# Kernel optimization log

Hardware: AMD Instinct MI355X
Metric: run time of the kernel (lower is better)

## Reference

```python
import jax, jax.numpy as jnp
import numpy as np
import math

B, C, IMG, K, N = 8, 3, 512, 4, 4

# ---- Simoncelli steerable-pyramid radial/angular filters (frequency domain) ----

def _L(r):
    # lowpass raised-cosine: 2 for r<=pi/4, 0 for r>=pi/2
    rc = np.clip(r, np.pi / 4, np.pi / 2)
    return 2.0 * np.cos(np.pi / 2 * np.log2(4.0 * rc / np.pi))

def _Hf(r):
    # highpass raised-cosine: 0 for r<=pi/4, 1 for r>=pi/2
    rc = np.clip(r, np.pi / 4, np.pi / 2)
    return np.cos(np.pi / 2 * np.log2(2.0 * rc / np.pi))

def _grid(H):
    # fftshifted rows (u in [-pi,pi)), rfft half-spectrum cols (v in [0,pi])
    u = (np.arange(H) - H // 2) * (2.0 * np.pi / H)
    v = np.arange(H // 2 + 1) * (2.0 * np.pi / H)
    U, V = np.meshgrid(u, v, indexing='ij')
    return np.sqrt(U * U + V * V), np.arctan2(U, V)

def _make_filters():
    H = IMG
    r, _ = _grid(H)
    # HL0_matrix: stack of H0=H(r/2) and L0=L(r/2)/2  -> [2, H, H//2+1]
    hl0 = np.stack([_Hf(r / 2.0), _L(r / 2.0) / 2.0]).astype(np.float32)
    aK = 2.0 ** (K - 1) * math.factorial(K - 1) / math.sqrt(K * math.factorial(2 * (K - 1)))
    bs, ls = [], []
    for n in range(N):
        r, t = _grid(H)
        hr = _Hf(r)
        # B_matrix: B_k = H(r) * aK * cos(theta - pi*k/K)^(K-1), angle wrapped mod pi into [-pi/2,pi/2)
        b = np.stack([hr * aK * np.cos(np.mod(t - np.pi * k / K + np.pi / 2, np.pi) - np.pi / 2) ** (K - 1)
                      for k in range(K)])
        bs.append(b.astype(np.float32))
        # L_matrix_cropped / 4: central crop of L(r) matching central_crop(lf)
        ls.append((_L(r)[H // 4:H // 4 + H // 2, :H // 4 + 1] / 4.0)[None].astype(np.float32))
        H //= 2
    return hl0, bs, ls

def setup_inputs() -> dict:
    key = jax.random.key(0)
    x = jax.random.normal(key, (B, C, IMG, IMG), dtype=jnp.float32)
    hl0, bs, ls = _make_filters()
    d = {"x": x, "hl0": jnp.asarray(hl0)}
    for n in range(N):
        d[f"b{n}"] = jnp.asarray(bs[n])
        d[f"l{n}"] = jnp.asarray(ls[n])
    return d

def _central_crop(z):
    H = z.shape[-2]
    return z[..., H // 4:H // 4 + H // 2, :H // 4 + 1]

def _forward(x, hl0, bs, ls):
    # complex half-spectrum replaces torch's (real, imag) channel pair; filters are real
    X = jnp.fft.fftshift(jnp.fft.rfft2(x), axes=-2)[..., None, :, :]  # [B,C,1,H,Wh] c64
    Y = hl0 * X                                                       # [B,C,2,H,Wh]
    h0f = Y[..., 0:1, :, :]
    lf = Y[..., 1:2, :, :]
    outs = []
    for n in range(N):
        bf = bs[n] * lf                     # [B,C,K,Hn,Whn]
        lf = ls[n] * _central_crop(lf)      # [B,C,1,Hn/2,Hn/4+1]
        if n == 0:
            bf = jnp.concatenate([h0f, bf], axis=-3)  # prepend highpass residual
        outs.append(bf)
    outs.append(lf)
    res = []
    for o in outs:
        o = jnp.fft.ifftshift(o, axes=-2)
        Hn = o.shape[-2]
        res.append(jnp.fft.irfft2(o, s=(Hn, Hn)))     # [B,C,feat,Hn,Hn]
    # includeHF: split highpass channel out of level-0 bands
    res = [res[0][..., 0:1, :, :], res[0][..., 1:, :, :]] + res[1:]
    return tuple(r[:, None] for r in res)             # each [B,1,C,feat,Hn,Hn]

def reference(x, hl0, b0, b1, b2, b3, l0, l1, l2, l3):
    return _forward(x, hl0, [b0, b1, b2, b3], [l0, l1, l2, l3])
```

## Files before the change

kernel.cpp:

```cpp
#include <hip/hip_runtime.h>
#include <hip/hip_bf16.h>


#define PI_F 3.14159265358979323846f

static __device__ inline float2 f2add(float2 a, float2 b){ return make_float2(a.x+b.x, a.y+b.y); }
static __device__ inline float2 f2sub(float2 a, float2 b){ return make_float2(a.x-b.x, a.y-b.y); }
static __device__ inline float2 cmul(float2 a, float2 b){ return make_float2(a.x*b.x - a.y*b.y, a.x*b.y + a.y*b.x); }

template<int N, bool INV>
static __device__ inline void fill_tw(float2* tw, int tid) {
    for (int m = tid; m < N; m += 256) {
        float ang = (INV ? 2.0f * PI_F : -2.0f * PI_F) * (float)m / (float)N;
        float s, c; __sincosf(ang, &s, &c);
        tw[m] = make_float2(c, s);
    }
}

template<int N, int F, bool INV>
static __device__ float2* fft_lds(float2* bufa, float2* bufb, const float2* tw, int tid) {
    constexpr int L = (N==512)?9:(N==256)?8:(N==128)?7:(N==64)?6:5;
    float2* src = bufa;
    float2* dst = bufb;
    if constexpr (L & 1) {
        __syncthreads();
        constexpr int NB = F * (N/2);
#pragma unroll
        for (int qq = 0; qq < NB; qq += 256) {
            int q = qq + tid;
            int f = q / (N/2), j = q % (N/2);
            float2 u = src[f*N + j];
            float2 v = src[f*N + j + N/2];
            dst[f*N + 2*j]     = f2add(u, v);
            dst[f*N + 2*j + 1] = f2sub(u, v);
        }
        float2* t = src; src = dst; dst = t;
    }
    constexpr int S4 = L / 2;
    constexpr int NB4 = F * (N/4);
#pragma unroll
    for (int s = 0; s < S4; ++s) {
        const int Ns = ((L & 1) ? 2 : 1) << (2*s);
        __syncthreads();
#pragma unroll
        for (int qq = 0; qq < NB4; qq += 256) {
            int q = qq + tid;
            int f = q / (N/4), j = q % (N/4);
            int r = j & (Ns - 1);
            int m = r * (N / (4*Ns));
            float2 w1 = tw[m];
            float2 w2 = tw[(2*m) & (N-1)];
            float2 w3 = tw[(3*m) & (N-1)];
            const float2* sp = src + f*N + j;
            float2 c0 = sp[0];
            float2 c1 = cmul(w1, sp[N/4]);
            float2 c2 = cmul(w2, sp[2*(N/4)]);
            float2 c3 = cmul(w3, sp[3*(N/4)]);
            float2 t0 = f2add(c0, c2), t1 = f2sub(c0, c2);
            float2 t2 = f2add(c1, c3), d  = f2sub(c1, c3);
            float2 t3 = INV ? make_float2(-d.y, d.x) : make_float2(d.y, -d.x);
            float2* dp = dst + f*N + (((j - r) << 2) | r);
            dp[0]      = f2add(t0, t2);
            dp[Ns]     = f2add(t1, t3);
            dp[2*Ns]   = f2sub(t0, t2);
            dp[3*Ns]   = f2sub(t1, t3);
        }
        float2* t = src; src = dst; dst = t;
    }
    __syncthreads();
    return src;
}

__global__ __launch_bounds__(256) void k_fwd_rows(const float* __restrict__ x,
                                                  float2* __restrict__ S) {
    __shared__ float2 lds[2][2*512];
    __shared__ float2 tw[512];
    int bid = blockIdx.x;
    int i = bid / 128, p = bid % 128;
    int y0 = 4 * p;
    const float* rbase = x + ((size_t)(i*512 + y0)) * 512;
    int tid = threadIdx.x;
    fill_tw<512,false>(tw, tid);
    for (int t = tid; t < 1024; t += 256) {
        int f = t / 512, idx = t % 512;
        lds[0][f*512 + idx] = make_float2(rbase[(size_t)(2*f)*512 + idx],
                                          rbase[(size_t)(2*f+1)*512 + idx]);
    }
    float2* res = fft_lds<512,2,false>(&lds[0][0], &lds[1][0], tw, tid);
    for (int t = tid; t < 2*257; t += 256) {
        int f = t / 257, v = t % 257;
        float2 Zv = res[f*512 + v];
        float2 Zc = res[f*512 + ((512 - v) & 511)];
        float2* SA = S + ((size_t)(i*512 + y0 + 2*f)) * 257;
        SA[v]       = make_float2(0.5f*(Zv.x + Zc.x), 0.5f*(Zv.y - Zc.y));
        SA[257 + v] = make_float2(0.5f*(Zv.y + Zc.y), 0.5f*(Zc.x - Zv.x));
    }
}

template<int N, int CB>
__global__ __launch_bounds__(256) void k_fwd_cols(float2* __restrict__ S, int nTiles) {
    constexpr int W = N/2 + 1;
    __shared__ float2 lds[2][CB*N];
    __shared__ float2 tw[N];
    int tid = threadIdx.x, bid = blockIdx.x;
    int i = bid / nTiles, v0 = (bid % nTiles) * CB;
    fill_tw<N,false>(tw, tid);
    float2* base = S + (size_t)i * N * W;
    for (int q = tid; q < CB*N; q += 256) {
        int c = q % CB, r = q / CB, v = v0 + c;
        lds[0][c*N + r] = (v < W) ? base[(size_t)r*W + v] : make_float2(0.f, 0.f);
    }
    float2* res = fft_lds<N, CB, false>(&lds[0][0], &lds[1][0], tw, tid);
    for (int q = tid; q < CB*N; q += 256) {
        int c = q % CB, r = q / CB, v = v0 + c;
        if (v < W) base[(size_t)r*W + v] = res[c*N + r];
    }
}

__global__ void k_lfall(const float2* __restrict__ S, const float* __restrict__ hl0,
                        const float* __restrict__ l0, const float* __restrict__ l1,
                        const float* __restrict__ l2, const float* __restrict__ l3,
                        float2* __restrict__ LF1, float2* __restrict__ LF2,
                        float2* __restrict__ LF3, float2* __restrict__ LF4) {
    const int P1 = 256*129, P2 = 128*65, P3 = 64*33, P4 = 32*17;
    const int T1 = 24*P1, T2 = 24*P2, T3 = 24*P3, T4 = 24*P4;
    int idx = blockIdx.x * 256 + threadIdx.x;
    int lev, rem, perim; float2* dst;
    if (idx < T1)                { lev = 1; rem = idx;              perim = P1; dst = LF1; }
    else if (idx < T1+T2)        { lev = 2; rem = idx - T1;        perim = P2; dst = LF2; }
    else if (idx < T1+T2+T3)     { lev = 3; rem = idx - T1 - T2;   perim = P3; dst = LF3; }
    else if (idx < T1+T2+T3+T4)  { lev = 4; rem = idx - T1-T2-T3;  perim = P4; dst = LF4; }
    else return;
    int i = rem / perim;
    int off = rem % perim;
    int Hn = 512 >> lev, Wn = Hn/2 + 1;
    int u = off / Wn, v = off % Wn;
    float f = 1.0f;
    for (int m = lev - 1; m >= 0; --m) {
        int Hc = 512 >> (m + 1);
        int Wc = Hc/2 + 1;
        int s2 = (u + Hc/2) & (Hc - 1);
        const float* ls = (m==0) ? l0 : (m==1) ? l1 : (m==2) ? l2 : l3;
        f *= ls[s2 * Wc + v];
        int Hp = 512 >> m;
        u = (3*(Hp/4) + s2) & (Hp - 1);
    }
    f *= hl0[512*257 + (((u + 256) & 511) * 257 + v)];
    float2 sv = S[((size_t)i * 512 + u) * 257 + v];
    dst[(size_t)i * perim + off] = make_float2(sv.x * f, sv.y * f);
}

template<int N, int CB, int MODE>
__global__ __launch_bounds__(256) void k_inv_cols(
        const float2* __restrict__ specA, const float2* __restrict__ specB,
        const float* __restrict__ filtA, const float* __restrict__ filtB, int filtStride,
        const float* __restrict__ filtH,
        float2* __restrict__ Z, int chOff, int nTiles) {
    constexpr int W = N/2 + 1;
    __shared__ float2 lds[2][CB*N];
    __shared__ float2 tw[N];
    int tid = threadIdx.x, bid = blockIdx.x, y = blockIdx.y;
    int i = bid / nTiles, v0 = (bid % nTiles) * CB;
    fill_tw<N,true>(tw, tid);
    const float2* spec = (y == 0) ? specA : specB;
    const float* filt = nullptr;
    if (MODE >= 1) filt = (y == 0) ? filtA : filtB + (size_t)(y - chOff) * filtStride;
    const float2* base = spec + (size_t)i * N * W;
    float2* Zb = Z + ((size_t)y * 24 + i) * N * W;
    for (int q = tid; q < CB*N; q += 256) {
        int c = q % CB, r = q / CB, v = v0 + c;
        float2 val = make_float2(0.f, 0.f);
        if (v < W) {
            val = base[(size_t)r*W + v];
            if (MODE >= 1) {
                int fi = ((r + N/2) & (N-1)) * W + v;
                float f = filt[fi];
                if (MODE == 2 && y > 0) f *= filtH[fi];
                val.x *= f; val.y *= f;
            }
        }
        lds[0][c*N + r] = val;
    }
    float2* res = fft_lds<N, CB, true>(&lds[0][0], &lds[1][0], tw, tid);
    for (int q = tid; q < CB*N; q += 256) {
        int c = q % CB, r = q / CB, v = v0 + c;
        if (v < W) Zb[(size_t)r*W + v] = res[c*N + r];
    }
}

template<int N, int RB>
__global__ __launch_bounds__(256) void k_irfft_rows(
        const float2* __restrict__ Z,
        float* __restrict__ outA, int CHA,
        float* __restrict__ outB, int CHB, int chOff, int rowBlocks) {
    constexpr int W = N/2 + 1;
    __shared__ float2 lds[2][RB*N];
    __shared__ float2 tw[N];
    int tid = threadIdx.x, bid = blockIdx.x, y = blockIdx.y;
    int i = bid / rowBlocks, u0 = (bid % rowBlocks) * RB;
    fill_tw<N,true>(tw, tid);
    const float2* Zb = Z + ((size_t)y * 24 + i) * N * W;
    float* outb; int CH, ch;
    if (y == 0) { outb = outA; CH = CHA; ch = 0; }
    else        { outb = outB; CH = CHB; ch = y - chOff; }
    for (int q = tid; q < RB*N; q += 256) {
        int f = q / N, p = q % N;
        const float2* Zr = Zb + (size_t)(u0 + f) * W;
        float2 val;
        if (p == 0)          { float2 t = Zr[0];     val = make_float2(t.x, 0.f); }
        else if (p < N/2)    { val = Zr[p]; }
        else if (p == N/2)   { float2 t = Zr[N/2];   val = make_float2(t.x, 0.f); }
        else                 { float2 t = Zr[N - p]; val = make_float2(t.x, -t.y); }
        lds[0][f*N + p] = val;
    }
    float2* res = fft_lds<N, RB, true>(&lds[0][0], &lds[1][0], tw, tid);
    constexpr float sc = 1.0f / ((float)N * (float)N);
    for (int q = tid; q < RB*N; q += 256) {
        int f = q / N, p = q % N;
        int u = u0 + f;
        outb[(((size_t)i * CH + ch) * N + u) * N + p] = res[f*N + p].x * sc;
    }
}

extern "C" void kernel_launch(void* const* d_in, const int* in_sizes, int n_in,
                              void* d_out, int out_size, void* d_ws, size_t ws_size,
                              hipStream_t stream) {
    auto find = [&](int sz) -> const float* {
        for (int t = 0; t < n_in; ++t)
            if (in_sizes[t] == sz) return (const float*)d_in[t];
        return nullptr;
    };
    const float* x   = find(6291456);
    const float* hl0 = find(263168);
    const float* b0f = find(526336);
    const float* l0f = find(33024);
    const float* b1f = find(132096);
    const float* l1f = find(8320);
    const float* b2f = find(33280);
    const float* l2f = find(2112);
    const float* b3f = find(8448);
    const float* l3f = find(544);
    float* out = (float*)d_out;
    if (!x || !hl0 || !b0f || !l0f || !b1f || !l1f || !b2f || !l2f || !b3f || !l3f) return;

    const size_t P0 = (size_t)512*257, P1 = (size_t)256*129, P2 = (size_t)128*65,
                 P3 = (size_t)64*33,  P4 = (size_t)32*17;
    char* w = (char*)d_ws;
    float2* S   = (float2*)w; w += 24*P0*8;
    float2* LF1 = (float2*)w; w += 24*P1*8;
    float2* LF2 = (float2*)w; w += 24*P2*8;
    float2* LF3 = (float2*)w; w += 24*P3*8;
    float2* LF4 = (float2*)w; w += 24*P4*8;
    float2* Zar = (float2*)w; w += 5*24*P0*8;
    if ((size_t)(w - (char*)d_ws) > ws_size) return;

    const float* hl0_hi = hl0 + 512*257;

    k_fwd_rows<<<dim3(24*128), 256, 0, stream>>>(x, S);
    k_fwd_cols<512,4><<<dim3(24*65), 256, 0, stream>>>(S, 65);

    k_lfall<<<dim3(4125), 256, 0, stream>>>(S, hl0, l0f, l1f, l2f, l3f, LF1, LF2, LF3, LF4);

    k_inv_cols<512,4,2><<<dim3(24*65, 5), 256, 0, stream>>>(S, S, hl0, b0f, (int)P0, hl0_hi, Zar, 1, 65);
    k_irfft_rows<512,4><<<dim3(24*128, 5), 256, 0, stream>>>(Zar, out + 0, 1, out + 6291456, 4, 1, 128);

    k_inv_cols<256,8,1><<<dim3(24*17, 4), 256, 0, stream>>>(LF1, LF1, b1f, b1f, (int)P1, nullptr, Zar, 0, 17);
    k_irfft_rows<256,8><<<dim3(24*32, 4), 256, 0, stream>>>(Zar, out + 31457280, 4, out + 31457280, 4, 0, 32);

    k_inv_cols<128,16,1><<<dim3(24*5, 4), 256, 0, stream>>>(LF2, LF2, b2f, b2f, (int)P2, nullptr, Zar, 0, 5);
    k_irfft_rows<128,16><<<dim3(24*8, 4), 256, 0, stream>>>(Zar, out + 37748736, 4, out + 37748736, 4, 0, 8);

    k_inv_cols<64,32,1><<<dim3(24*2, 4), 256, 0, stream>>>(LF3, LF3, b3f, b3f, (int)P3, nullptr, Zar, 0, 2);
    k_irfft_rows<64,32><<<dim3(24*2, 4), 256, 0, stream>>>(Zar, out + 39321600, 4, out + 39321600, 4, 0, 2);

    k_inv_cols<32,64,0><<<dim3(24*1, 1), 256, 0, stream>>>(LF4, LF4, nullptr, nullptr, 0, nullptr, Zar, 0, 1);
    k_irfft_rows<32,32><<<dim3(24*1, 1), 256, 0, stream>>>(Zar, out + 39714816, 1, out + 39714816, 1, 0, 1);

    (void)out_size; (void)ws_size;
}
```

Before: 605.8 us.

## Use in-place padded LDS FFT, padded spectrum rows, and split level-0 inverse

Replaces the ping-pong LDS FFT with an in-place variant: each stage loads its operands into registers, synchronises, then writes back, using a padded LDS index (one extra slot every 16 elements) to reduce bank conflicts. Global spectrum rows are padded to 16-element-aligned widths (272, 144, ...) so column accesses line up better. Column FFT tiles are unified at 8 columns. The level-0 inverse is split into 3+2 channel launches so the Z scratch only needs 3 planes. The in-place FFT adds an extra barrier per stage and more registers, and the split adds launches.

```diff
diff --git a/kernel.cpp b/kernel.cpp
--- a/kernel.cpp
+++ b/kernel.cpp
@@ -7,6 +7,8 @@
 static __device__ inline float2 f2add(float2 a, float2 b){ return make_float2(a.x+b.x, a.y+b.y); }
 static __device__ inline float2 f2sub(float2 a, float2 b){ return make_float2(a.x-b.x, a.y-b.y); }
 static __device__ inline float2 cmul(float2 a, float2 b){ return make_float2(a.x*b.x - a.y*b.y, a.x*b.y + a.y*b.x); }
+
+#define PIDX(p) ((p) + ((p) >> 4))
 
 template<int N, bool INV>
 static __device__ inline void fill_tw(float2* tw, int tid) {
@@ -18,102 +20,131 @@
 }
 
 template<int N, int F, bool INV>
-static __device__ float2* fft_lds(float2* bufa, float2* bufb, const float2* tw, int tid) {
+static __device__ void fft_reg(float2* __restrict__ buf, const float2* __restrict__ tw, int tid) {
     constexpr int L = (N==512)?9:(N==256)?8:(N==128)?7:(N==64)?6:5;
-    float2* src = bufa;
-    float2* dst = bufb;
+    constexpr int STR = N + (N>>4) + 1;
     if constexpr (L & 1) {
+        constexpr int NB2 = F*(N/2);
+        constexpr int PT2 = (NB2 + 255)/256;
+        constexpr bool G2 = (NB2 % 256) != 0;
+        float2 ra[PT2], rb[PT2];
         __syncthreads();
-        constexpr int NB = F * (N/2);
-#pragma unroll
-        for (int qq = 0; qq < NB; qq += 256) {
-            int q = qq + tid;
-            int f = q / (N/2), j = q % (N/2);
-            float2 u = src[f*N + j];
-            float2 v = src[f*N + j + N/2];
-            dst[f*N + 2*j]     = f2add(u, v);
-            dst[f*N + 2*j + 1] = f2sub(u, v);
-        }
-        float2* t = src; src = dst; dst = t;
-    }
-    constexpr int S4 = L / 2;
-    constexpr int NB4 = F * (N/4);
+#pragma unroll
+        for (int t = 0; t < PT2; ++t) {
+            int q = t*256 + tid;
+            if (!G2 || q < NB2) {
+                int f = q / (N/2), j = q % (N/2);
+                ra[t] = buf[f*STR + PIDX(j)];
+                rb[t] = buf[f*STR + PIDX(j + N/2)];
+            }
+        }
+        __syncthreads();
+#pragma unroll
+        for (int t = 0; t < PT2; ++t) {
+            int q = t*256 + tid;
+            if (!G2 || q < NB2) {
+                int f = q / (N/2), j = q % (N/2);
+                buf[f*STR + PIDX(2*j)]   = f2add(ra[t], rb[t]);
+                buf[f*STR + PIDX(2*j+1)] = f2sub(ra[t], rb[t]);
+            }
+        }
+    }
+    constexpr int S4  = L/2;
+    constexpr int NB4 = F*(N/4);
+    constexpr int PT4 = (NB4 + 255)/256;
+    constexpr bool G4 = (NB4 % 256) != 0;
 #pragma unroll
     for (int s = 0; s < S4; ++s) {
         const int Ns = ((L & 1) ? 2 : 1) << (2*s);
+        float2 c0[PT4], c1[PT4], c2[PT4], c3[PT4];
         __syncthreads();
 #pragma unroll
-        for (int qq = 0; qq < NB4; qq += 256) {
-            int q = qq + tid;
-            int f = q / (N/4), j = q % (N/4);
-            int r = j & (Ns - 1);
-            int m = r * (N / (4*Ns));
-            float2 w1 = tw[m];
-            float2 w2 = tw[(2*m) & (N-1)];
-            float2 w3 = tw[(3*m) & (N-1)];
-            const float2* sp = src + f*N + j;
-            float2 c0 = sp[0];
-            float2 c1 = cmul(w1, sp[N/4]);
-            float2 c2 = cmul(w2, sp[2*(N/4)]);
-            float2 c3 = cmul(w3, sp[3*(N/4)]);
-            float2 t0 = f2add(c0, c2), t1 = f2sub(c0, c2);
-            float2 t2 = f2add(c1, c3), d  = f2sub(c1, c3);
-            float2 t3 = INV ? make_float2(-d.y, d.x) : make_float2(d.y, -d.x);
-            float2* dp = dst + f*N + (((j - r) << 2) | r);
-            dp[0]      = f2add(t0, t2);
-            dp[Ns]     = f2add(t1, t3);
-            dp[2*Ns]   = f2sub(t0, t2);
-            dp[3*Ns]   = f2sub(t1, t3);
-        }
-        float2* t = src; src = dst; dst = t;
+        for (int t = 0; t < PT4; ++t) {
+            int q = t*256 + tid;
+            if (!G4 || q < NB4) {
+                int f = q / (N/4), j = q % (N/4);
+                float2* b = buf + f*STR;
+                c0[t] = b[PIDX(j)];
+                c1[t] = b[PIDX(j + (N/4))];
+                c2[t] = b[PIDX(j + 2*(N/4))];
+                c3[t] = b[PIDX(j + 3*(N/4))];
+            }
+        }
+        __syncthreads();
+#pragma unroll
+        for (int t = 0; t < PT4; ++t) {
+            int q = t*256 + tid;
+            if (!G4 || q < NB4) {
+                int f = q / (N/4), j = q % (N/4);
+                int r = j & (Ns - 1);
+                int m = r * (N / (4*Ns));
+                float2 w1 = tw[m];
+                float2 w2 = tw[(2*m) & (N-1)];
+                float2 w3 = tw[(3*m) & (N-1)];
+                float2 d0 = c0[t];
+                float2 d1 = cmul(w1, c1[t]);
+                float2 d2 = cmul(w2, c2[t]);
+                float2 d3 = cmul(w3, c3[t]);
+                float2 t0 = f2add(d0, d2), t1 = f2sub(d0, d2);
+                float2 t2 = f2add(d1, d3), dd = f2sub(d1, d3);
+                float2 t3 = INV ? make_float2(-dd.y, dd.x) : make_float2(dd.y, -dd.x);
+                float2* b = buf + f*STR;
+                int d = ((j - r) << 2) | r;
+                b[PIDX(d)]        = f2add(t0, t2);
+                b[PIDX(d + Ns)]   = f2add(t1, t3);
+                b[PIDX(d + 2*Ns)] = f2sub(t0, t2);
+                b[PIDX(d + 3*Ns)] = f2sub(t1, t3);
+            }
+        }
     }
     __syncthreads();
-    return src;
 }
 
 __global__ __launch_bounds__(256) void k_fwd_rows(const float* __restrict__ x,
                                                   float2* __restrict__ S) {
-    __shared__ float2 lds[2][2*512];
+    constexpr int STR = 512 + 32 + 1;
+    __shared__ float2 buf[2*STR];
     __shared__ float2 tw[512];
     int bid = blockIdx.x;
     int i = bid / 128, p = bid % 128;
-    int y0 = 4 * p;
+    int y0 = 4*p;
     const float* rbase = x + ((size_t)(i*512 + y0)) * 512;
     int tid = threadIdx.x;
     fill_tw<512,false>(tw, tid);
     for (int t = tid; t < 1024; t += 256) {
-        int f = t / 512, idx = t % 512;
-        lds[0][f*512 + idx] = make_float2(rbase[(size_t)(2*f)*512 + idx],
-                                          rbase[(size_t)(2*f+1)*512 + idx]);
-    }
-    float2* res = fft_lds<512,2,false>(&lds[0][0], &lds[1][0], tw, tid);
+        int f = t >> 9, idx = t & 511;
+        buf[f*STR + PIDX(idx)] = make_float2(rbase[(size_t)(2*f)*512 + idx],
+                                             rbase[(size_t)(2*f+1)*512 + idx]);
+    }
+    fft_reg<512,2,false>(buf, tw, tid);
     for (int t = tid; t < 2*257; t += 256) {
         int f = t / 257, v = t % 257;
-        float2 Zv = res[f*512 + v];
-        float2 Zc = res[f*512 + ((512 - v) & 511)];
-        float2* SA = S + ((size_t)(i*512 + y0 + 2*f)) * 257;
+        float2 Zv = buf[f*STR + PIDX(v)];
+        float2 Zc = buf[f*STR + PIDX((512 - v) & 511)];
+        float2* SA = S + ((size_t)(i*512 + y0 + 2*f)) * 272;
         SA[v]       = make_float2(0.5f*(Zv.x + Zc.x), 0.5f*(Zv.y - Zc.y));
-        SA[257 + v] = make_float2(0.5f*(Zv.y + Zc.y), 0.5f*(Zc.x - Zv.x));
-    }
-}
-
-template<int N, int CB>
+        SA[272 + v] = make_float2(0.5f*(Zv.y + Zc.y), 0.5f*(Zc.x - Zv.x));
+    }
+}
+
+template<int N>
 __global__ __launch_bounds__(256) void k_fwd_cols(float2* __restrict__ S, int nTiles) {
-    constexpr int W = N/2 + 1;
-    __shared__ float2 lds[2][CB*N];
+    constexpr int W = N/2 + 1, WP = N/2 + 16;
+    constexpr int STR = N + (N>>4) + 1;
+    __shared__ float2 buf[8*STR];
     __shared__ float2 tw[N];
     int tid = threadIdx.x, bid = blockIdx.x;
-    int i = bid / nTiles, v0 = (bid % nTiles) * CB;
+    int i = bid / nTiles, v0 = (bid % nTiles) * 8;
     fill_tw<N,false>(tw, tid);
-    float2* base = S + (size_t)i * N * W;
-    for (int q = tid; q < CB*N; q += 256) {
-        int c = q % CB, r = q / CB, v = v0 + c;
-        lds[0][c*N + r] = (v < W) ? base[(size_t)r*W + v] : make_float2(0.f, 0.f);
-    }
-    float2* res = fft_lds<N, CB, false>(&lds[0][0], &lds[1][0], tw, tid);
-    for (int q = tid; q < CB*N; q += 256) {
-        int c = q % CB, r = q / CB, v = v0 + c;
-        if (v < W) base[(size_t)r*W + v] = res[c*N + r];
+    float2* base = S + (size_t)i * N * WP;
+    for (int q = tid; q < 8*N; q += 256) {
+        int c = q & 7, r = q >> 3, v = v0 + c;
+        buf[c*STR + PIDX(r)] = (v < W) ? base[(size_t)r*WP + v] : make_float2(0.f,0.f);
+    }
+    fft_reg<N,8,false>(buf, tw, tid);
+    for (int q = tid; q < 8*N; q += 256) {
+        int c = q & 7, r = q >> 3, v = v0 + c;
+        if (v < W) base[(size_t)r*WP + v] = buf[c*STR + PIDX(r)];
     }
 }
 
@@ -122,19 +153,20 @@
                         const float* __restrict__ l2, const float* __restrict__ l3,
                         float2* __restrict__ LF1, float2* __restrict__ LF2,
                         float2* __restrict__ LF3, float2* __restrict__ LF4) {
-    const int P1 = 256*129, P2 = 128*65, P3 = 64*33, P4 = 32*17;
-    const int T1 = 24*P1, T2 = 24*P2, T3 = 24*P3, T4 = 24*P4;
+    const int D1 = 256*129, D2 = 128*65, D3 = 64*33, D4 = 32*17;
+    const int T1 = 24*D1, T2 = 24*D2, T3 = 24*D3, T4 = 24*D4;
     int idx = blockIdx.x * 256 + threadIdx.x;
-    int lev, rem, perim; float2* dst;
-    if (idx < T1)                { lev = 1; rem = idx;              perim = P1; dst = LF1; }
-    else if (idx < T1+T2)        { lev = 2; rem = idx - T1;        perim = P2; dst = LF2; }
-    else if (idx < T1+T2+T3)     { lev = 3; rem = idx - T1 - T2;   perim = P3; dst = LF3; }
-    else if (idx < T1+T2+T3+T4)  { lev = 4; rem = idx - T1-T2-T3;  perim = P4; dst = LF4; }
+    int lev, rem; float2* dst; int Wnp;
+    if (idx < T1)               { lev=1; rem=idx;          dst=LF1; Wnp=144; }
+    else if (idx < T1+T2)       { lev=2; rem=idx-T1;       dst=LF2; Wnp=80; }
+    else if (idx < T1+T2+T3)    { lev=3; rem=idx-T1-T2;    dst=LF3; Wnp=48; }
+    else if (idx < T1+T2+T3+T4) { lev=4; rem=idx-T1-T2-T3; dst=LF4; Wnp=32; }
     else return;
-    int i = rem / perim;
-    int off = rem % perim;
     int Hn = 512 >> lev, Wn = Hn/2 + 1;
-    int u = off / Wn, v = off % Wn;
+    int dper = Hn * Wn;
+    int i = rem / dper, off = rem % dper;
+    int uo = off / Wn, v = off % Wn;
+    int u = uo;
     float f = 1.0f;
     for (int m = lev - 1; m >= 0; --m) {
         int Hc = 512 >> (m + 1);
@@ -146,45 +178,51 @@
         u = (3*(Hp/4) + s2) & (Hp - 1);
     }
     f *= hl0[512*257 + (((u + 256) & 511) * 257 + v)];
-    float2 sv = S[((size_t)i * 512 + u) * 257 + v];
-    dst[(size_t)i * perim + off] = make_float2(sv.x * f, sv.y * f);
-}
-
-template<int N, int CB, int MODE>
+    float2 sv = S[((size_t)i * 512 + u) * 272 + v];
+    dst[((size_t)i * Hn + uo) * Wnp + v] = make_float2(sv.x * f, sv.y * f);
+}
+
+template<int N, int MODE>
 __global__ __launch_bounds__(256) void k_inv_cols(
-        const float2* __restrict__ specA, const float2* __restrict__ specB,
-        const float* __restrict__ filtA, const float* __restrict__ filtB, int filtStride,
-        const float* __restrict__ filtH,
-        float2* __restrict__ Z, int chOff, int nTiles) {
-    constexpr int W = N/2 + 1;
-    __shared__ float2 lds[2][CB*N];
+        const float2* __restrict__ spec,
+        const float* __restrict__ filtA, const float* __restrict__ filtB,
+        const float* __restrict__ filtH, int filtStride, int yBase,
+        float2* __restrict__ Z, int nTiles) {
+    constexpr int W = N/2 + 1, WP = N/2 + 16;
+    constexpr int STR = N + (N>>4) + 1;
+    __shared__ float2 buf[8*STR];
     __shared__ float2 tw[N];
     int tid = threadIdx.x, bid = blockIdx.x, y = blockIdx.y;
-    int i = bid / nTiles, v0 = (bid % nTiles) * CB;
+    int i = bid / nTiles, v0 = (bid % nTiles) * 8;
+    int eff = y + yBase;
     fill_tw<N,true>(tw, tid);
-    const float2* spec = (y == 0) ? specA : specB;
     const float* filt = nullptr;
-    if (MODE >= 1) filt = (y == 0) ? filtA : filtB + (size_t)(y - chOff) * filtStride;
-    const float2* base = spec + (size_t)i * N * W;
-    float2* Zb = Z + ((size_t)y * 24 + i) * N * W;
-    for (int q = tid; q < CB*N; q += 256) {
-        int c = q % CB, r = q / CB, v = v0 + c;
+    bool useH = false;
+    if (MODE == 1) filt = filtB + (size_t)eff * filtStride;
+    if (MODE == 2) {
+        if (eff == 0) filt = filtA;
+        else { filt = filtB + (size_t)(eff - 1) * filtStride; useH = true; }
+    }
+    const float2* base = spec + (size_t)i * N * WP;
+    float2* Zb = Z + ((size_t)y * 24 + i) * N * WP;
+    for (int q = tid; q < 8*N; q += 256) {
+        int c = q & 7, r = q >> 3, v = v0 + c;
         float2 val = make_float2(0.f, 0.f);
         if (v < W) {
-            val = base[(size_t)r*W + v];
+            val = base[(size_t)r*WP + v];
             if (MODE >= 1) {
                 int fi = ((r + N/2) & (N-1)) * W + v;
                 float f = filt[fi];
-                if (MODE == 2 && y > 0) f *= filtH[fi];
+                if (MODE == 2 && useH) f *= filtH[fi];
                 val.x *= f; val.y *= f;
             }
         }
-        lds[0][c*N + r] = val;
-    }
-    float2* res = fft_lds<N, CB, true>(&lds[0][0], &lds[1][0], tw, tid);
-    for (int q = tid; q < CB*N; q += 256) {
-        int c = q % CB, r = q / CB, v = v0 + c;
-        if (v < W) Zb[(size_t)r*W + v] = res[c*N + r];
+        buf[c*STR + PIDX(r)] = val;
+    }
+    fft_reg<N,8,true>(buf, tw, tid);
+    for (int q = tid; q < 8*N; q += 256) {
+        int c = q & 7, r = q >> 3, v = v0 + c;
+        if (v < W) Zb[(size_t)r*WP + v] = buf[c*STR + PIDX(r)];
     }
 }
 
@@ -192,33 +230,35 @@
 __global__ __launch_bounds__(256) void k_irfft_rows(
         const float2* __restrict__ Z,
         float* __restrict__ outA, int CHA,
-        float* __restrict__ outB, int CHB, int chOff, int rowBlocks) {
-    constexpr int W = N/2 + 1;
-    __shared__ float2 lds[2][RB*N];
+        float* __restrict__ outB, int CHB,
+        int chOff, int yBase, int rowBlocks) {
+    constexpr int WP = N/2 + 16;
+    constexpr int STR = N + (N>>4) + 1;
+    __shared__ float2 buf[RB*STR];
     __shared__ float2 tw[N];
     int tid = threadIdx.x, bid = blockIdx.x, y = blockIdx.y;
     int i = bid / rowBlocks, u0 = (bid % rowBlocks) * RB;
+    int eff = y + yBase;
     fill_tw<N,true>(tw, tid);
-    const float2* Zb = Z + ((size_t)y * 24 + i) * N * W;
+    const float2* Zb = Z + ((size_t)y * 24 + i) * N * WP;
     float* outb; int CH, ch;
-    if (y == 0) { outb = outA; CH = CHA; ch = 0; }
-    else        { outb = outB; CH = CHB; ch = y - chOff; }
+    if (eff == 0) { outb = outA; CH = CHA; ch = 0; }
+    else          { outb = outB; CH = CHB; ch = eff - chOff; }
     for (int q = tid; q < RB*N; q += 256) {
         int f = q / N, p = q % N;
-        const float2* Zr = Zb + (size_t)(u0 + f) * W;
+        const float2* Zr = Zb + (size_t)(u0 + f) * WP;
         float2 val;
         if (p == 0)          { float2 t = Zr[0];     val = make_float2(t.x, 0.f); }
         else if (p < N/2)    { val = Zr[p]; }
         else if (p == N/2)   { float2 t = Zr[N/2];   val = make_float2(t.x, 0.f); }
         else                 { float2 t = Zr[N - p]; val = make_float2(t.x, -t.y); }
-        lds[0][f*N + p] = val;
-    }
-    float2* res = fft_lds<N, RB, true>(&lds[0][0], &lds[1][0], tw, tid);
+        buf[f*STR + PIDX(p)] = val;
+    }
+    fft_reg<N,RB,true>(buf, tw, tid);
     constexpr float sc = 1.0f / ((float)N * (float)N);
     for (int q = tid; q < RB*N; q += 256) {
         int f = q / N, p = q % N;
-        int u = u0 + f;
-        outb[(((size_t)i * CH + ch) * N + u) * N + p] = res[f*N + p].x * sc;
+        outb[(((size_t)i * CH + ch) * N + (u0 + f)) * N + p] = buf[f*STR + PIDX(p)].x * sc;
     }
 }
 
@@ -243,38 +283,40 @@
     float* out = (float*)d_out;
     if (!x || !hl0 || !b0f || !l0f || !b1f || !l1f || !b2f || !l2f || !b3f || !l3f) return;
 
-    const size_t P0 = (size_t)512*257, P1 = (size_t)256*129, P2 = (size_t)128*65,
-                 P3 = (size_t)64*33,  P4 = (size_t)32*17;
+    const size_t P0p = (size_t)512*272, P1p = (size_t)256*144, P2p = (size_t)128*80,
+                 P3p = (size_t)64*48,  P4p = (size_t)32*32;
     char* w = (char*)d_ws;
-    float2* S   = (float2*)w; w += 24*P0*8;
-    float2* LF1 = (float2*)w; w += 24*P1*8;
-    float2* LF2 = (float2*)w; w += 24*P2*8;
-    float2* LF3 = (float2*)w; w += 24*P3*8;
-    float2* LF4 = (float2*)w; w += 24*P4*8;
-    float2* Zar = (float2*)w; w += 5*24*P0*8;
+    float2* S   = (float2*)w; w += 24*P0p*8;
+    float2* LF1 = (float2*)w; w += 24*P1p*8;
+    float2* LF2 = (float2*)w; w += 24*P2p*8;
+    float2* LF3 = (float2*)w; w += 24*P3p*8;
+    float2* LF4 = (float2*)w; w += 24*P4p*8;
+    float2* Zar = (float2*)w; w += 3*24*P0p*8;
     if ((size_t)(w - (char*)d_ws) > ws_size) return;
 
     const float* hl0_hi = hl0 + 512*257;
 
     k_fwd_rows<<<dim3(24*128), 256, 0, stream>>>(x, S);
-    k_fwd_cols<512,4><<<dim3(24*65), 256, 0, stream>>>(S, 65);
+    k_fwd_cols<512><<<dim3(24*33), 256, 0, stream>>>(S, 33);
 
     k_lfall<<<dim3(4125), 256, 0, stream>>>(S, hl0, l0f, l1f, l2f, l3f, LF1, LF2, LF3, LF4);
 
-    k_inv_cols<512,4,2><<<dim3(24*65, 5), 256, 0, stream>>>(S, S, hl0, b0f, (int)P0, hl0_hi, Zar, 1, 65);
-    k_irfft_rows<512,4><<<dim3(24*128, 5), 256, 0, stream>>>(Zar, out + 0, 1, out + 6291456, 4, 1, 128);
-
-    k_inv_cols<256,8,1><<<dim3(24*17, 4), 256, 0, stream>>>(LF1, LF1, b1f, b1f, (int)P1, nullptr, Zar, 0, 17);
-    k_irfft_rows<256,8><<<dim3(24*32, 4), 256, 0, stream>>>(Zar, out + 31457280, 4, out + 31457280, 4, 0, 32);
-
-    k_inv_cols<128,16,1><<<dim3(24*5, 4), 256, 0, stream>>>(LF2, LF2, b2f, b2f, (int)P2, nullptr, Zar, 0, 5);
-    k_irfft_rows<128,16><<<dim3(24*8, 4), 256, 0, stream>>>(Zar, out + 37748736, 4, out + 37748736, 4, 0, 8);
-
-    k_inv_cols<64,32,1><<<dim3(24*2, 4), 256, 0, stream>>>(LF3, LF3, b3f, b3f, (int)P3, nullptr, Zar, 0, 2);
-    k_irfft_rows<64,32><<<dim3(24*2, 4), 256, 0, stream>>>(Zar, out + 39321600, 4, out + 39321600, 4, 0, 2);
-
-    k_inv_cols<32,64,0><<<dim3(24*1, 1), 256, 0, stream>>>(LF4, LF4, nullptr, nullptr, 0, nullptr, Zar, 0, 1);
-    k_irfft_rows<32,32><<<dim3(24*1, 1), 256, 0, stream>>>(Zar, out + 39714816, 1, out + 39714816, 1, 0, 1);
+    k_inv_cols<512,2><<<dim3(24*33, 3), 256, 0, stream>>>(S, hl0, b0f, hl0_hi, 512*257, 0, Zar, 33);
+    k_irfft_rows<512,4><<<dim3(24*128, 3), 256, 0, stream>>>(Zar, out, 1, out + 6291456, 4, 1, 0, 128);
+    k_inv_cols<512,2><<<dim3(24*33, 2), 256, 0, stream>>>(S, hl0, b0f, hl0_hi, 512*257, 3, Zar, 33);
+    k_irfft_rows<512,4><<<dim3(24*128, 2), 256, 0, stream>>>(Zar, out, 1, out + 6291456, 4, 1, 3, 128);
+
+    k_inv_cols<256,1><<<dim3(24*17, 4), 256, 0, stream>>>(LF1, nullptr, b1f, nullptr, 256*129, 0, Zar, 17);
+    k_irfft_rows<256,8><<<dim3(24*32, 4), 256, 0, stream>>>(Zar, out + 31457280, 4, out + 31457280, 4, 0, 0, 32);
+
+    k_inv_cols<128,1><<<dim3(24*9, 4), 256, 0, stream>>>(LF2, nullptr, b2f, nullptr, 128*65, 0, Zar, 9);
+    k_irfft_rows<128,16><<<dim3(24*8, 4), 256, 0, stream>>>(Zar, out + 37748736, 4, out + 37748736, 4, 0, 0, 8);
+
+    k_inv_cols<64,1><<<dim3(24*5, 4), 256, 0, stream>>>(LF3, nullptr, b3f, nullptr, 64*33, 0, Zar, 5);
+    k_irfft_rows<64,32><<<dim3(24*2, 4), 256, 0, stream>>>(Zar, out + 39321600, 4, out + 39321600, 4, 0, 0, 2);
+
+    k_inv_cols<32,0><<<dim3(24*3, 1), 256, 0, stream>>>(LF4, nullptr, nullptr, nullptr, 0, 0, Zar, 3);
+    k_irfft_rows<32,32><<<dim3(24, 1), 256, 0, stream>>>(Zar, out + 39714816, 1, out + 39714816, 1, 0, 0, 1);
 
     (void)out_size; (void)ws_size;
 }
```

After: 490.9 us. -19.0%, faster.
